# Kernel optimization log

Measured on AMD Instinct MI355X. Metric: run time of the kernel, lower is better.

## Reference

```python
import jax, jax.numpy as jnp
import numpy as np

N_MET, N_RXN, N_GENE = 2534, 4881, 6607
E, P, D = 262144, 131072, 256
LN_EPS = 1e-5


def _segment_mean(x, idx, n):
    s = jax.ops.segment_sum(x, idx, num_segments=n)
    c = jax.ops.segment_sum(jnp.ones((idx.shape[0],), x.dtype), idx, num_segments=n)
    return s / jnp.maximum(c, 1.0)[:, None]


def _hyperconv(x, eattr, node, edge, stoich, W, We, att, b):
    # PyG-style HypergraphConv with stoichiometry as incidence weight + attention.
    xp = x @ W                      # [N_MET, D]
    ep = eattr @ We                 # [N_RXN, D]
    xi = xp[node]                   # [E, D] gather
    ej = ep[edge]                   # [E, D] gather
    logits = jax.nn.leaky_relu(jnp.concatenate([xi, ej], axis=-1) @ att, 0.2)  # [E]
    m = jax.ops.segment_max(logits, edge, num_segments=N_RXN)
    ex = jnp.exp(logits - m[edge])
    ssum = jax.ops.segment_sum(ex, edge, num_segments=N_RXN)
    alpha = ex / (ssum[edge] + 1e-16)           # softmax per hyperedge
    w = stoich * alpha                           # [E]
    ones = jnp.ones_like(stoich)
    Bc = jax.ops.segment_sum(ones, edge, num_segments=N_RXN)   # nodes per edge
    me = jax.ops.segment_sum(w[:, None] * xi, edge, num_segments=N_RXN)
    me = me / jnp.maximum(Bc, 1.0)[:, None]      # node -> hyperedge
    Dc = jax.ops.segment_sum(ones, node, num_segments=N_MET)   # edges per node
    out = jax.ops.segment_sum(w[:, None] * me[edge], node, num_segments=N_MET)
    out = out / jnp.maximum(Dc, 1.0)[:, None]    # hyperedge -> node
    return out + b


def _layernorm(z, g, b):
    mu = jnp.mean(z, axis=-1, keepdims=True)
    var = jnp.mean(jnp.square(z - mu), axis=-1, keepdims=True)
    return (z - mu) / jnp.sqrt(var + LN_EPS) * g + b


def _renorm(emb):
    # nn.Embedding(max_norm=1.0): clamp row norms to <= 1
    n = jnp.linalg.norm(emb, axis=-1, keepdims=True)
    return emb * jnp.minimum(1.0, 1.0 / (n + 1e-12))


def setup_inputs() -> dict:
    key = jax.random.key(0)
    ks = jax.random.split(key, 16)
    s = 1.0 / np.sqrt(D)
    return {
        "he_node": jax.random.randint(ks[0], (E,), 0, N_MET),
        "he_edge": jax.random.randint(ks[1], (E,), 0, N_RXN),
        "stoich": jax.random.normal(ks[2], (E,), dtype=jnp.float32),
        "gene_x": jax.random.normal(ks[3], (N_GENE, D), dtype=jnp.float32),
        "rtg_rxn": jax.random.randint(ks[4], (P,), 0, N_RXN),
        "rtg_gene": jax.random.randint(ks[5], (P,), 0, N_GENE),
        "emb_table": jax.random.normal(ks[6], (N_MET, D), dtype=jnp.float32) * 0.02,
        "W0": jax.random.normal(ks[7], (D, D), dtype=jnp.float32) * s,
        "We0": jax.random.normal(ks[8], (D, D), dtype=jnp.float32) * s,
        "att0": jax.random.normal(ks[9], (2 * D,), dtype=jnp.float32) * s,
        "b0": jnp.zeros((D,), jnp.float32),
        "W1": jax.random.normal(ks[10], (D, D), dtype=jnp.float32) * s,
        "We1": jax.random.normal(ks[11], (D, D), dtype=jnp.float32) * s,
        "att1": jax.random.normal(ks[12], (2 * D,), dtype=jnp.float32) * s,
        "b1": jnp.zeros((D,), jnp.float32),
        "ln_g": jnp.ones((D,), jnp.float32),
        "ln_b": jnp.zeros((D,), jnp.float32),
    }


def reference(he_node, he_edge, stoich, gene_x, rtg_rxn, rtg_gene, emb_table,
              W0, We0, att0, b0, W1, We1, att1, b1, ln_g, ln_b):
    met = _renorm(emb_table)                                    # [N_MET, D]
    # gene -> reaction scatter-mean (flattened reaction_to_genes dict)
    rxn_emb = _segment_mean(gene_x[rtg_gene], rtg_rxn, N_RXN)   # [N_RXN, D]
    # layer 0 (no skip on first layer)
    cur = jnp.tanh(_hyperconv(met, rxn_emb, he_node, he_edge, stoich, W0, We0, att0, b0))
    # layer 1 with skip + layernorm
    nxt = jnp.tanh(_hyperconv(cur, rxn_emb, he_node, he_edge, stoich, W1, We1, att1, b1))
    cur = _layernorm(nxt + cur, ln_g, ln_b)
    # metabolite -> reaction scatter-mean over incidences
    rxn_final = _segment_mean(cur[he_node], he_edge, N_RXN)     # [N_RXN, D]
    # reaction -> gene scatter-mean
    gene_emb = _segment_mean(rxn_final[rtg_rxn], rtg_gene, N_GENE)  # [N_GENE, D]
    return gene_emb
```

## Files before the change

kernel.cpp:

```cpp
#include <hip/hip_runtime.h>
#include <math.h>

#define DD 256
static constexpr int N_MET  = 2534;
static constexpr int N_RXN  = 4881;
static constexpr int N_GENE = 6607;
static constexpr int NE     = 262144;
static constexpr int NP     = 131072;

static constexpr int NCHUNK = 256;
static constexpr int NCHG   = 128;
static constexpr int NBE    = 77;
static constexpr int NBN    = 80;
static constexpr int NBG    = 104;
static constexpr int CHS    = 80;
static constexpr int NCOL   = NBE + NBN + NBG;
static constexpr int GEMM_BLOCKS = (N_MET + 15) / 16;
static constexpr int KP2_GEMM0 = NBE + NBN + NBG;

__device__ __forceinline__ float waveSum(float v) {
  #pragma unroll
  for (int o = 32; o > 0; o >>= 1) v += __shfl_xor(v, o, 64);
  return v;
}
__device__ __forceinline__ float waveMax(float v) {
  #pragma unroll
  for (int o = 32; o > 0; o >>= 1) v = fmaxf(v, __shfl_xor(v, o, 64));
  return v;
}
__device__ __forceinline__ int   bcasti(int v, int l)   { return __builtin_amdgcn_readlane(v, l); }
__device__ __forceinline__ float bcastf(float v, int l) {
  return __int_as_float(__builtin_amdgcn_readlane(__float_as_int(v), l));
}

__global__ __launch_bounds__(1024) void KH_k(
    const int* __restrict__ he_node, const int* __restrict__ he_edge,
    const int* __restrict__ rtg_rxn, const int* __restrict__ rtg_gene,
    int* cntR,
    int* __restrict__ chE, int* __restrict__ chN, int* __restrict__ chG,
    const float* __restrict__ We0, const float* __restrict__ att0,
    const float* __restrict__ We1, const float* __restrict__ att1,
    float* __restrict__ ve0, float* __restrict__ ve1) {
  int blk = blockIdx.x, tid = threadIdx.x;
  if (blk < 32) {
    int wid = blk * 16 + (tid >> 6);
    int lane = tid & 63;
    const float* We = (wid < 256) ? We0 : We1;
    const float* at = (wid < 256) ? att0 : att1;
    int r = wid & 255;
    float4 a = ((const float4*)(We + (size_t)r * DD))[lane];
    float4 v = ((const float4*)(at + DD))[lane];
    float s = waveSum(a.x * v.x + a.y * v.y + a.z * v.z + a.w * v.w);
    if (lane == 0) ((wid < 256) ? ve0 : ve1)[r] = s;
    return;
  }
  int c = blk - 32;
  __shared__ int hE[NBE], hN[NBN], hG[NBG];
  if (tid < NBE) hE[tid] = 0;
  if (tid >= 128 && tid < 128 + NBN) hN[tid - 128] = 0;
  if (tid >= 256 && tid < 256 + NBG) hG[tid - 256] = 0;
  __syncthreads();
  int i = c * 1024 + tid;
  int n = he_node[i], e = he_edge[i];
  atomicAdd(&hE[e >> 6], 1); atomicAdd(&hN[n >> 5], 1);
  if (c < NCHG) {
    int r = rtg_rxn[i], g = rtg_gene[i];
    atomicAdd(&cntR[r], 1);
    atomicAdd(&hG[g >> 6], 1);
  }
  __syncthreads();
  if (tid < NBE) chE[c * CHS + tid] = hE[tid];
  if (tid >= 128 && tid < 128 + NBN) chN[c * CHS + (tid - 128)] = hN[tid - 128];
  if (c < NCHG && tid >= 256 && tid < 256 + NBG) chG[c * NBG + (tid - 256)] = hG[tid - 256];
}

__global__ __launch_bounds__(1024) void KScan_k(
    int* __restrict__ chE, int* __restrict__ chN, int* __restrict__ chG,
    int* __restrict__ totE, int* __restrict__ totN, int* __restrict__ totG,
    const float* __restrict__ gene_x,
    const float* __restrict__ ve0, const float* __restrict__ ve1,
    float* __restrict__ gdot0, float* __restrict__ gdot1) {
  int blk = blockIdx.x, tid = threadIdx.x;
  if (blk < 17) {
    int colw = blk * 16 + (tid >> 6);
    int lane = tid & 63;
// ... 52 lines not shown
}

__global__ __launch_bounds__(1024) void KP1_k(
    const int* __restrict__ he_node, const int* __restrict__ he_edge,
    const float* __restrict__ stoich,
    const int* __restrict__ chE, const int* __restrict__ chN,
    const int* __restrict__ chG,
    const int* __restrict__ totE, const int* __restrict__ totN,
    const int* __restrict__ totG,
    int2* __restrict__ scrE, int2* __restrict__ scrN, int* __restrict__ scrG,
    const int* __restrict__ rtg_rxn, const int* __restrict__ rtg_gene,
    const float* __restrict__ gdot0, const float* __restrict__ gdot1,
    float* __restrict__ seAcc0, float* __restrict__ seAcc1) {
  int c = blockIdx.x, tid = threadIdx.x;
  __shared__ int sc[128];
  __shared__ int cursE[NBE], cursN[NBN], cursG[NBG];
  int v;
  if (tid < 128) sc[tid] = (tid < NBE) ? totE[tid] : 0;
  if (tid < 128) v = sc[tid];
  __syncthreads();
  ldsScan128(sc, tid);
  if (tid < NBE) cursE[tid] = (sc[tid] - v) + chE[c * CHS + tid];
  __syncthreads();
  if (tid < 128) sc[tid] = (tid < NBN) ? totN[tid] : 0;
  if (tid < 128) v = sc[tid];
  __syncthreads();
  ldsScan128(sc, tid);
  if (tid < NBN) cursN[tid] = (sc[tid] - v) + chN[c * CHS + tid];
  __syncthreads();
  if (c < NCHG) {
    if (tid < 128) sc[tid] = (tid < NBG) ? totG[tid] : 0;
    if (tid < 128) v = sc[tid];
    __syncthreads();
    ldsScan128(sc, tid);
    if (tid < NBG) cursG[tid] = (sc[tid] - v) + chG[c * NBG + tid];
  }
  __syncthreads();
  int i = c * 1024 + tid;
  int n = he_node[i], e = he_edge[i];
  int st = __float_as_int(stoich[i]);
  int dE = atomicAdd(&cursE[e >> 6], 1);
  scrE[dE] = make_int2((e << 12) | n, st);
  int dN = atomicAdd(&cursN[n >> 5], 1);
  scrN[dN] = make_int2((n << 13) | e, st);
  if (c < NCHG) {
    int r = rtg_rxn[i], g = rtg_gene[i];
    int dG = atomicAdd(&cursG[g >> 6], 1);
    scrG[dG] = (g << 13) | r;
    atomicAdd(&seAcc0[r], gdot0[g]);
    atomicAdd(&seAcc1[r], gdot1[g]);
  }
}

template <bool RENORM>
__device__ __forceinline__ void gemm_body(const float* __restrict__ X,
                                          const float* __restrict__ W,
                                          const float* __restrict__ att,
                                          float* __restrict__ Y,
                                          float* __restrict__ sn, int M, int r0) {
  __shared__ float Xs[256][20];
  __shared__ float red[4][16];
  __shared__ float scl[16];
  int tid = threadIdx.x;
  int w = tid >> 6, lane = tid & 63;
  float xv[16];
  #pragma unroll
  for (int i = 0; i < 16; ++i) {
    int r = r0 + i;
    xv[i] = (r < M) ? X[(size_t)r * DD + tid] : 0.f;
  }
  if (RENORM) {
    #pragma unroll
    for (int i = 0; i < 16; ++i) {
      float v = waveSum(xv[i] * xv[i]);
      if (lane == 0) red[w][i] = v;
    }
    __syncthreads();
    if (tid < 16) {
      float t = red[0][tid] + red[1][tid] + red[2][tid] + red[3][tid];
      scl[tid] = fminf(1.f, 1.f / (sqrtf(t) + 1e-12f));
    }
    __syncthreads();
    #pragma unroll
    for (int i = 0; i < 16; ++i) xv[i] *= scl[i];
  }
  #pragma unroll
  for (int i = 0; i < 16; ++i) Xs[tid][i] = xv[i];
  __syncthreads();
  float acc[16];
  #pragma unroll
  for (int i = 0; i < 16; ++i) acc[i] = 0.f;
  const float* wp = W + tid;
  #pragma unroll 8
  for (int k = 0; k < 256; ++k) {
    float wv = wp[(size_t)k * DD];
    const float4* xr = reinterpret_cast<const float4*>(&Xs[k][0]);
    float4 a0 = xr[0], a1 = xr[1], a2 = xr[2], a3 = xr[3];
    acc[0]  += a0.x * wv; acc[1]  += a0.y * wv; acc[2]  += a0.z * wv; acc[3]  += a0.w * wv;
    acc[4]  += a1.x * wv; acc[5]  += a1.y * wv; acc[6]  += a1.z * wv; acc[7]  += a1.w * wv;
    acc[8]  += a2.x * wv; acc[9]  += a2.y * wv; acc[10] += a2.z * wv; acc[11] += a2.w * wv;
    acc[12] += a3.x * wv; acc[13] += a3.y * wv; acc[14] += a3.z * wv; acc[15] += a3.w * wv;
  }
  #pragma unroll
  for (int i = 0; i < 16; ++i) {
    int r = r0 + i;
    if (r < M) Y[(size_t)r * DD + tid] = acc[i];
  }
  float av = att[tid];
  __syncthreads();
  #pragma unroll
  for (int i = 0; i < 16; ++i) {
    float v = waveSum(acc[i] * av);
    if (lane == 0) red[w][i] = v;
  }
  __syncthreads();
  if (tid < 16) {
    int r = r0 + tid;
    if (r < M) sn[r] = red[0][tid] + red[1][tid] + red[2][tid] + red[3][tid];
  }
}

__device__ __forceinline__ int blockSumInt256(int v) {
  __shared__ int s4[4];
  #pragma unroll
  for (int o = 32; o > 0; o >>= 1) v += __shfl_xor(v, o, 64);
  if ((threadIdx.x & 63) == 0) s4[threadIdx.x >> 6] = v;
  __syncthreads();
  return s4[0] + s4[1] + s4[2] + s4[3];
}

__global__ __launch_bounds__(256) void KP2_k(
    const int* __restrict__ totE, const int* __restrict__ totN,
    const int* __restrict__ totG,
    const int2* __restrict__ scrE, const int2* __restrict__ scrN,
    const int* __restrict__ scrG,
    int* __restrict__ offsE, int* __restrict__ offsN, int* __restrict__ offsG,
    int2* __restrict__ payE, int2* __restrict__ payN, int* __restrict__ rxnG,
    const float* __restrict__ emb, const float* __restrict__ W0,
    const float* __restrict__ att0, float* __restrict__ xp, float* __restrict__ sn) {
  int blk = blockIdx.x, tid = threadIdx.x;
  if (blk >= KP2_GEMM0) {
    gemm_body<true>(emb, W0, att0, xp, sn, N_MET, (blk - KP2_GEMM0) * 16);
    return;
  }
  __shared__ int cnt[64];
  __shared__ int curs[64];
  int side, b, klo, kcnt, nk, btot;
  const int* tot;
  if (blk < NBE)            { side = 0; b = blk;             tot = totE; klo = 64 * b; nk = N_RXN;  kcnt = min(64, N_RXN  - klo); }
  else if (blk < NBE + NBN) { side = 1; b = blk - NBE;       tot = totN; klo = 32 * b; nk = N_MET;  kcnt = min(32, N_MET  - klo); }
  else                      { side = 2; b = blk - NBE - NBN; tot = totG; klo = 64 * b; nk = N_GENE; kcnt = min(64, N_GENE - klo); }
  btot = tot[b];
  int pv = (tid < b) ? tot[tid] : 0;
  int base = blockSumInt256(pv);
  if (tid < 64) cnt[tid] = 0;
  __syncthreads();
  int lo = base, hi = base + btot;
  for (int j = lo + tid; j < hi; j += 256) {
    int key;
    if (side == 0)      key = (scrE[j].x >> 12) - klo;
    else if (side == 1) key = (scrN[j].x >> 13) - klo;
    else                key = (scrG[j]   >> 13) - klo;
    atomicAdd(&cnt[key], 1);
  }
  __syncthreads();
  if (tid < 64) {
    int v = cnt[tid];
    int inc = v;
    #pragma unroll
    for (int o = 1; o < 64; o <<= 1) { int t = __shfl_up(inc, o, 64); if (tid >= o) inc += t; }
    int ex = inc - v;
    curs[tid] = base + ex;
    int* offs = (side == 0) ? offsE : (side == 1) ? offsN : offsG;
    if (tid < kcnt) offs[klo + tid] = base + ex;
    if (tid == 0 && klo + kcnt == nk) offs[nk] = base + btot;
  }
  __syncthreads();
  for (int j = lo + tid; j < hi; j += 256) {
    if (side == 0) {
      int2 r = scrE[j];
      int e = r.x >> 12, n = r.x & 4095;
      int slot = atomicAdd(&curs[e - klo], 1);
      payE[slot] = make_int2(n, r.y);
    } else if (side == 1) {
      int2 r = scrN[j];
      int n = r.x >> 13, e = r.x & 8191;
      int slot = atomicAdd(&curs[n - klo], 1);
      payN[slot] = make_int2(e, r.y);
    } else {
      int pw = scrG[j];
      int g = pw >> 13, rr = pw & 8191;
      int slot = atomicAdd(&curs[g - klo], 1);
      rxnG[slot] = rr;
    }
  }
}

__global__ __launch_bounds__(256) void gemm1_k(const float* __restrict__ X,
                                               const float* __restrict__ W,
                                               const float* __restrict__ att,
                                               float* __restrict__ Y,
                                               float* __restrict__ sn, int M) {
  gemm_body<false>(X, W, att, Y, sn, M, blockIdx.x * 16);
}

__device__ __forceinline__ void gatherAcc(float4& acc, const float4* __restrict__ src4,
                                          const int (&rv)[4], const float (&wv)[4],
                                          int nc, int lane) {
  #pragma unroll
  for (int c = 0; c < 4; ++c) {
    int lim = nc - c * 64; if (lim > 64) lim = 64;
    for (int t = 0; t < lim; t += 16) {
      float4 a[16]; float w[16];
      #pragma unroll
      for (int q = 0; q < 16; ++q) {
        int   n = bcasti(rv[c], t + q);
        w[q]    = bcastf(wv[c], t + q);
        a[q]    = src4[(size_t)n * 64 + lane];
      }
      #pragma unroll
      for (int q = 0; q < 16; ++q) {
        acc.x += w[q] * a[q].x; acc.y += w[q] * a[q].y;
        acc.z += w[q] * a[q].z; acc.w += w[q] * a[q].w;
      }
    }
  }
}

__device__ __forceinline__ void gatherAcc2(float2& acc, const float2* __restrict__ src2,
                                           const int (&rv)[4], const float (&wv)[4],
                                           int nc, int fbase) {
  #pragma unroll
  for (int c = 0; c < 4; ++c) {
    int lim = nc - c * 64; if (lim > 64) lim = 64;
    for (int t = 0; t < lim; t += 16) {
      float2 a[16]; float w[16];
      #pragma unroll
      for (int q = 0; q < 16; ++q) {
        int   n = bcasti(rv[c], t + q);
        w[q]    = bcastf(wv[c], t + q);
        a[q]    = src2[(size_t)n * 128 + fbase];
      }
      #pragma unroll
      for (int q = 0; q < 16; ++q) {
        acc.x += w[q] * a[q].x; acc.y += w[q] * a[q].y;
      }
    }
  }
}

template <int STRIDE>
__global__ __launch_bounds__(256) void seg_mean_k(const int* __restrict__ offs,
                                                  const int* __restrict__ pay,
                                                  const float* __restrict__ src,
                                                  float* __restrict__ dst, int nseg) {
  int wid = (blockIdx.x * 256 + threadIdx.x) >> 6;
  int lane = threadIdx.x & 63;
  if (wid >= nseg) return;
  int beg = offs[wid], end = offs[wid + 1];
  int cnt = end - beg;
  int nc = cnt < 256 ? cnt : 256;
  int rv[4]; float wv[4];
  #pragma unroll
  for (int c = 0; c < 4; ++c) {
    int j = c * 64 + lane;
    if (j < nc) { rv[c] = pay[(size_t)(beg + j) * STRIDE]; wv[c] = 1.f; }
    else        { rv[c] = 0;                               wv[c] = 0.f; }
  }
  float4 acc = make_float4(0.f, 0.f, 0.f, 0.f);
  gatherAcc(acc, (const float4*)src, rv, wv, nc, lane);
  for (int j = 256; j < cnt; ++j) {
    int n = pay[(size_t)(beg + j) * STRIDE];
    float4 a = ((const float4*)src)[(size_t)n * 64 + lane];
    acc.x += a.x; acc.y += a.y; acc.z += a.z; acc.w += a.w;
  }
  float inv = 1.f / (float)(cnt > 1 ? cnt : 1);
  float4 o; o.x = acc.x * inv; o.y = acc.y * inv; o.z = acc.z * inv; o.w = acc.w * inv;
  ((float4*)dst)[(size_t)wid * 64 + lane] = o;
}

__global__ __launch_bounds__(256) void me_k(const int* __restrict__ offs,
                                            const int2* __restrict__ payE,
                                            const float* __restrict__ sn,
                                            const float* __restrict__ seAcc,
                                            const int* __restrict__ cntR,
                                            const float* __restrict__ xp,
                                            float* __restrict__ me,
                                            float4* __restrict__ rstat) {
  int gw = (blockIdx.x * 256 + threadIdx.x) >> 6;
  int wid = gw >> 1, half = gw & 1;
  int lane = threadIdx.x & 63;
  if (wid >= N_RXN) return;
  int rc = cntR[wid];
  float ser = seAcc[wid] / (float)(rc > 1 ? rc : 1);

  int beg = offs[wid], end = offs[wid + 1];
  int cnt = end - beg;
  int nc = cnt < 256 ? cnt : 256;
  int nv[4]; float wv[4]; float stv[4];
  float lmax = -1e30f;
  #pragma unroll
  for (int c = 0; c < 4; ++c) {
    int j = c * 64 + lane;
    if (j < nc) {
      int2 p = payE[beg + j];
      float l = sn[p.x] + ser;
      l = (l >= 0.f) ? l : 0.2f * l;
      nv[c] = p.x; wv[c] = l; stv[c] = __int_as_float(p.y);
      lmax = fmaxf(lmax, l);
    } else { nv[c] = 0; wv[c] = -1e30f; stv[c] = 0.f; }
  }
  for (int j = 256 + lane; j < cnt; j += 64) {
    int2 p = payE[beg + j];
    float l = sn[p.x] + ser;
    l = (l >= 0.f) ? l : 0.2f * l;
    lmax = fmaxf(lmax, l);
  }
  float m = waveMax(lmax);
  float s = 0.f;
  #pragma unroll
  for (int c = 0; c < 4; ++c) {
    if (c * 64 + lane < nc) { float e = expf(wv[c] - m); wv[c] = e; s += e; }
    else wv[c] = 0.f;
  }
  for (int j = 256 + lane; j < cnt; j += 64) {
    int2 p = payE[beg + j];
    float l = sn[p.x] + ser;
    l = (l >= 0.f) ? l : 0.2f * l;
    s += expf(l - m);
  }
  s = waveSum(s);
  float invS = 1.f / (s + 1e-16f);
  #pragma unroll
  for (int c = 0; c < 4; ++c) {
    if (c * 64 + lane < nc) wv[c] = stv[c] * wv[c] * invS;
  }
  if (half == 0 && lane == 0) rstat[wid] = make_float4(ser, m, invS, 0.f);
  int fbase = half * 64 + lane;
  float2 acc = make_float2(0.f, 0.f);
  gatherAcc2(acc, (const float2*)xp, nv, wv, nc, fbase);
  for (int j = 256; j < cnt; ++j) {
    int2 p = payE[beg + j];
    float l = sn[p.x] + ser;
    l = (l >= 0.f) ? l : 0.2f * l;
    float w = __int_as_float(p.y) * expf(l - m) * invS;
    float2 a = ((const float2*)xp)[(size_t)p.x * 128 + fbase];
    acc.x += w * a.x; acc.y += w * a.y;
  }
  float invB = 1.f / (float)(cnt > 1 ? cnt : 1);
  float2 o; o.x = acc.x * invB; o.y = acc.y * invB;
  ((float2*)me)[(size_t)wid * 128 + fbase] = o;
}

template <bool LN>
__global__ __launch_bounds__(256) void out_k(const int* __restrict__ offs,
                                             const int2* __restrict__ payN,
                                             const float* __restrict__ sn,
                                             const float4* __restrict__ rstat,
                                             const float* __restrict__ me,
                                             const float* __restrict__ bias,
                                             const float* __restrict__ ln_g,
                                             const float* __restrict__ ln_b,
                                             float* __restrict__ cur) {
  int wid = (blockIdx.x * 256 + threadIdx.x) >> 6;
  int lane = threadIdx.x & 63;
  if (wid >= N_MET) return;
  int beg = offs[wid], end = offs[wid + 1];
  int cnt = end - beg;
  int nc = cnt < 256 ? cnt : 256;
  float sn_n = sn[wid];
  int rv[4]; float wv[4];
  #pragma unroll
  for (int c = 0; c < 4; ++c) {
    int j = c * 64 + lane;
    if (j < nc) {
      int2 p = payN[beg + j];
      float4 st = rstat[p.x];
      float l = sn_n + st.x;
      l = (l >= 0.f) ? l : 0.2f * l;
      rv[c] = p.x;
      wv[c] = __int_as_float(p.y) * expf(l - st.y) * st.z;
    } else { rv[c] = 0; wv[c] = 0.f; }
  }
  float4 acc = make_float4(0.f, 0.f, 0.f, 0.f);
  gatherAcc(acc, (const float4*)me, rv, wv, nc, lane);
  for (int j = 256; j < cnt; ++j) {
    int2 p = payN[beg + j];
    float4 st = rstat[p.x];
    float l = sn_n + st.x;
    l = (l >= 0.f) ? l : 0.2f * l;
    float w = __int_as_float(p.y) * expf(l - st.y) * st.z;
    float4 a = ((const float4*)me)[(size_t)p.x * 64 + lane];
    acc.x += w * a.x; acc.y += w * a.y; acc.z += w * a.z; acc.w += w * a.w;
  }
  float invD = 1.f / (float)(cnt > 1 ? cnt : 1);
  float4 b4 = ((const float4*)bias)[lane];
  float4 o;
  o.x = tanhf(acc.x * invD + b4.x);
  o.y = tanhf(acc.y * invD + b4.y);
  o.z = tanhf(acc.z * invD + b4.z);
  o.w = tanhf(acc.w * invD + b4.w);
  float4* cur4 = (float4*)cur;
  if (!LN) {
    cur4[(size_t)wid * 64 + lane] = o;
    return;
  }
  float4 p = cur4[(size_t)wid * 64 + lane];
  float4 z; z.x = o.x + p.x; z.y = o.y + p.y; z.z = o.z + p.z; z.w = o.w + p.w;
  float mu = waveSum(z.x + z.y + z.z + z.w) * (1.f / 256.f);
  float4 zc; zc.x = z.x - mu; zc.y = z.y - mu; zc.z = z.z - mu; zc.w = z.w - mu;
  float var = waveSum(zc.x * zc.x + zc.y * zc.y + zc.z * zc.z + zc.w * zc.w) * (1.f / 256.f);
  float rs = 1.f / sqrtf(var + 1e-5f);
  float4 g4 = ((const float4*)ln_g)[lane];
  float4 be4 = ((const float4*)ln_b)[lane];
  float4 r;
  r.x = zc.x * rs * g4.x + be4.x;
  r.y = zc.y * rs * g4.y + be4.y;
  r.z = zc.z * rs * g4.z + be4.z;
  r.w = zc.w * rs * g4.w + be4.w;
  cur4[(size_t)wid * 64 + lane] = r;
}

extern "C" void kernel_launch(void* const* d_in, const int* in_sizes, int n_in,
                              void* d_out, int out_size, void* d_ws, size_t ws_size,
                              hipStream_t stream) {
  const int*   he_node = (const int*)d_in[0];
  const int*   he_edge = (const int*)d_in[1];
  const float* stoich  = (const float*)d_in[2];
  const float* gene_x  = (const float*)d_in[3];
  const int*   rtg_rxn = (const int*)d_in[4];
  const int*   rtg_gene= (const int*)d_in[5];
  const float* emb     = (const float*)d_in[6];
  const float* W0      = (const float*)d_in[7];
  const float* We0     = (const float*)d_in[8];
  const float* att0    = (const float*)d_in[9];
  const float* b0      = (const float*)d_in[10];
  const float* W1      = (const float*)d_in[11];
  const float* We1     = (const float*)d_in[12];
  const float* att1    = (const float*)d_in[13];
  const float* b1      = (const float*)d_in[14];
  const float* ln_g    = (const float*)d_in[15];
  const float* ln_b    = (const float*)d_in[16];
  float* out = (float*)d_out;

  char* base = (char*)d_ws;
  size_t off = 0;
  auto carve = [&](size_t bytes) -> char* {
    char* p = base + off;
    off += (bytes + 255) & ~(size_t)255;
    return p;
  };
  float*  xp    = (float*)carve((size_t)N_MET * DD * 4);
  float*  me    = (float*)carve((size_t)N_RXN * DD * 4);
  float*  cur   = (float*)carve((size_t)N_MET * DD * 4);
  float*  rxnf  = (float*)carve((size_t)N_RXN * DD * 4);
  float*  sn    = (float*)carve((size_t)N_MET * 4);
  float*  ve0   = (float*)carve(DD * 4);
  float*  ve1   = (float*)carve(DD * 4);
  float*  gdot0 = (float*)carve((size_t)N_GENE * 4);
  float*  gdot1 = (float*)carve((size_t)N_GENE * 4);
  float4* rstat = (float4*)carve((size_t)N_RXN * 16);
  int ztot = 3 * N_RXN;
  int* zbase = (int*)carve((size_t)ztot * 4);
  int*   cntR   = zbase;
  float* seAcc0 = (float*)(cntR + N_RXN);
  float* seAcc1 = seAcc0 + N_RXN;
  int*  offsE = (int*)carve((N_RXN + 1) * 4);
  int2* payE  = (int2*)carve((size_t)NE * 8);
  int*  offsN = (int*)carve((N_MET + 1) * 4);
  int2* payN  = (int2*)carve((size_t)NE * 8);
  int*  offsG = (int*)carve((N_GENE + 1) * 4);
  int*  rxnG  = (int*)carve((size_t)NP * 4);
  int2* scrE  = (int2*)carve((size_t)NE * 8);
  int2* scrN  = (int2*)carve((size_t)NE * 8);
  int*  scrG  = (int*)carve((size_t)NP * 4);
  int*  chE   = (int*)carve((size_t)NCHUNK * CHS * 4);
  int*  chN   = (int*)carve((size_t)NCHUNK * CHS * 4);
  int*  chG   = (int*)carve((size_t)NCHG * NBG * 4);
  int*  totE  = (int*)carve(128 * 4);
  int*  totN  = (int*)carve(128 * 4);
  int*  totG  = (int*)carve(128 * 4);

  hipMemsetAsync(zbase, 0, (size_t)ztot * 4, stream);

  KH_k<<<32 + NCHUNK, 1024, 0, stream>>>(
      he_node, he_edge, rtg_rxn, rtg_gene, cntR,
      chE, chN, chG, We0, att0, We1, att1, ve0, ve1);

  int gdot_blocks = (N_GENE + 15) / 16;
  KScan_k<<<17 + gdot_blocks, 1024, 0, stream>>>(
      chE, chN, chG, totE, totN, totG, gene_x, ve0, ve1, gdot0, gdot1);

  KP1_k<<<NCHUNK, 1024, 0, stream>>>(
      he_node, he_edge, stoich, chE, chN, chG, totE, totN, totG,
      scrE, scrN, scrG, rtg_rxn, rtg_gene, gdot0, gdot1, seAcc0, seAcc1);

  KP2_k<<<KP2_GEMM0 + GEMM_BLOCKS, 256, 0, stream>>>(
      totE, totN, totG, scrE, scrN, scrG,
      offsE, offsN, offsG, payE, payN, rxnG,
      emb, W0, att0, xp, sn);

  me_k<<<(2 * N_RXN + 3) / 4, 256, 0, stream>>>(offsE, payE, sn, seAcc0, cntR,
                                                xp, me, rstat);
  out_k<false><<<(N_MET + 3) / 4, 256, 0, stream>>>(offsN, payN, sn, rstat, me, b0,
                                                    nullptr, nullptr, cur);

  gemm1_k<<<GEMM_BLOCKS, 256, 0, stream>>>(cur, W1, att1, xp, sn, N_MET);
  me_k<<<(2 * N_RXN + 3) / 4, 256, 0, stream>>>(offsE, payE, sn, seAcc1, cntR,
                                                xp, me, rstat);
  out_k<true><<<(N_MET + 3) / 4, 256, 0, stream>>>(offsN, payN, sn, rstat, me, b1,
                                                   ln_g, ln_b, cur);

  seg_mean_k<2><<<(N_RXN + 3) / 4, 256, 0, stream>>>(offsE, (const int*)payE, cur, rxnf, N_RXN);
  seg_mean_k<1><<<(N_GENE + 3) / 4, 256, 0, stream>>>(offsG, rxnG, rxnf, out, N_GENE);
}
```

Baseline: 221.8 us.

## Assign one block per segment and split incidences across four waves

```diff
diff --git a/kernel.cpp b/kernel.cpp
--- a/kernel.cpp
+++ b/kernel.cpp
@@ -31,6 +31,22 @@
 __device__ __forceinline__ int   bcasti(int v, int l)   { return __builtin_amdgcn_readlane(v, l); }
 __device__ __forceinline__ float bcastf(float v, int l) {
   return __int_as_float(__builtin_amdgcn_readlane(__float_as_int(v), l));
+}
+__device__ __forceinline__ float blockMax4(float v, float* red, int w, int lane) {
+  v = waveMax(v);
+  if (lane == 0) red[w] = v;
+  __syncthreads();
+  float r = fmaxf(fmaxf(red[0], red[1]), fmaxf(red[2], red[3]));
+  __syncthreads();
+  return r;
+}
+__device__ __forceinline__ float blockSum4(float v, float* red, int w, int lane) {
+  v = waveSum(v);
+  if (lane == 0) red[w] = v;
+  __syncthreads();
+  float r = red[0] + red[1] + red[2] + red[3];
+  __syncthreads();
+  return r;
 }
 
 __global__ __launch_bounds__(1024) void KH_k(
@@ -341,12 +357,12 @@
   gemm_body<false>(X, W, att, Y, sn, M, blockIdx.x * 16);
 }
 
-__device__ __forceinline__ void gatherAcc(float4& acc, const float4* __restrict__ src4,
-                                          const int (&rv)[4], const float (&wv)[4],
-                                          int nc, int lane) {
+__device__ __forceinline__ void gatherWave(float4& acc, const float4* __restrict__ src4,
+                                           const int (&rv)[4], const float (&wv)[4],
+                                           int jn, int lane) {
   #pragma unroll
   for (int c = 0; c < 4; ++c) {
-    int lim = nc - c * 64; if (lim > 64) lim = 64;
+    int lim = jn - c * 64; if (lim > 64) lim = 64;
     for (int t = 0; t < lim; t += 16) {
       float4 a[16]; float w[16];
       #pragma unroll
@@ -364,154 +380,124 @@
   }
 }
 
-__device__ __forceinline__ void gatherAcc2(float2& acc, const float2* __restrict__ src2,
-                                           const int (&rv)[4], const float (&wv)[4],
-                                           int nc, int fbase) {
-  #pragma unroll
-  for (int c = 0; c < 4; ++c) {
-    int lim = nc - c * 64; if (lim > 64) lim = 64;
-    for (int t = 0; t < lim; t += 16) {
-      float2 a[16]; float w[16];
-      #pragma unroll
-      for (int q = 0; q < 16; ++q) {
-        int   n = bcasti(rv[c], t + q);
-        w[q]    = bcastf(wv[c], t + q);
-        a[q]    = src2[(size_t)n * 128 + fbase];
-      }
-      #pragma unroll
-      for (int q = 0; q < 16; ++q) {
-        acc.x += w[q] * a[q].x; acc.y += w[q] * a[q].y;
-      }
-    }
-  }
-}
-
-template <int STRIDE>
-__global__ __launch_bounds__(256) void seg_mean_k(const int* __restrict__ offs,
-                                                  const int* __restrict__ pay,
-                                                  const float* __restrict__ src,
-                                                  float* __restrict__ dst, int nseg) {
-  int wid = (blockIdx.x * 256 + threadIdx.x) >> 6;
-  int lane = threadIdx.x & 63;
-  if (wid >= nseg) return;
-  int beg = offs[wid], end = offs[wid + 1];
+__device__ __forceinline__ bool combine4(float4& acc, float4 (*lacc)[64], int w, int lane) {
+  if (w > 0) lacc[w - 1][lane] = acc;
+  __syncthreads();
+  if (w == 0) {
+    float4 a1 = lacc[0][lane], a2 = lacc[1][lane], a3 = lacc[2][lane];
+    acc.x += a1.x + a2.x + a3.x;
+    acc.y += a1.y + a2.y + a3.y;
+    acc.z += a1.z + a2.z + a3.z;
+    acc.w += a1.w + a2.w + a3.w;
+    return true;
+  }
+  return false;
+}
+
+__global__ __launch_bounds__(256) void me_blk_k(const int* __restrict__ offs,
+                                                const int2* __restrict__ payE,
+                                                const float* __restrict__ sn,
+                                                const float* __restrict__ seAcc,
+                                                const int* __restrict__ cntR,
+                                                const float* __restrict__ xp,
+                                                float* __restrict__ me,
+                                                float4* __restrict__ rstat) {
+  __shared__ float red[4];
+  __shared__ float4 lacc[3][64];
+  int r = blockIdx.x;
+  int tid = threadIdx.x, w = tid >> 6, lane = tid & 63;
+  int beg = offs[r], end = offs[r + 1];
   int cnt = end - beg;
-  int nc = cnt < 256 ? cnt : 256;
-  int rv[4]; float wv[4];
+  int rc = cntR[r];
+  float ser = seAcc[r] / (float)(rc > 1 ? rc : 1);
+  int cap = cnt < 1024 ? cnt : 1024;
+  int q = (cap + 3) >> 2;
+  int jb = w * q;
+  int jn = cap - jb; if (jn < 0) jn = 0; if (jn > q) jn = q;
+  int nv[4]; float wv[4], stv[4];
+  float lmax = -1e30f;
   #pragma unroll
   for (int c = 0; c < 4; ++c) {
     int j = c * 64 + lane;
-    if (j < nc) { rv[c] = pay[(size_t)(beg + j) * STRIDE]; wv[c] = 1.f; }
-    else        { rv[c] = 0;                               wv[c] = 0.f; }
-  }
-  float4 acc = make_float4(0.f, 0.f, 0.f, 0.f);
-  gatherAcc(acc, (const float4*)src, rv, wv, nc, lane);
-  for (int j = 256; j < cnt; ++j) {
-    int n = pay[(size_t)(beg + j) * STRIDE];
-    float4 a = ((const float4*)src)[(size_t)n * 64 + lane];
-    acc.x += a.x; acc.y += a.y; acc.z += a.z; acc.w += a.w;
-  }
-  float inv = 1.f / (float)(cnt > 1 ? cnt : 1);
-  float4 o; o.x = acc.x * inv; o.y = acc.y * inv; o.z = acc.z * inv; o.w = acc.w * inv;
-  ((float4*)dst)[(size_t)wid * 64 + lane] = o;
-}
-
-__global__ __launch_bounds__(256) void me_k(const int* __restrict__ offs,
-                                            const int2* __restrict__ payE,
-                                            const float* __restrict__ sn,
-                                            const float* __restrict__ seAcc,
-                                            const int* __restrict__ cntR,
-                                            const float* __restrict__ xp,
-                                            float* __restrict__ me,
-                                            float4* __restrict__ rstat) {
-  int gw = (blockIdx.x * 256 + threadIdx.x) >> 6;
-  int wid = gw >> 1, half = gw & 1;
-  int lane = threadIdx.x & 63;
-  if (wid >= N_RXN) return;
-  int rc = cntR[wid];
-  float ser = seAcc[wid] / (float)(rc > 1 ? rc : 1);
-
-  int beg = offs[wid], end = offs[wid + 1];
-  int cnt = end - beg;
-  int nc = cnt < 256 ? cnt : 256;
-  int nv[4]; float wv[4]; float stv[4];
-  float lmax = -1e30f;
-  #pragma unroll
-  for (int c = 0; c < 4; ++c) {
-    int j = c * 64 + lane;
-    if (j < nc) {
-      int2 p = payE[beg + j];
+    if (j < jn) {
+      int2 p = payE[beg + jb + j];
       float l = sn[p.x] + ser;
       l = (l >= 0.f) ? l : 0.2f * l;
       nv[c] = p.x; wv[c] = l; stv[c] = __int_as_float(p.y);
       lmax = fmaxf(lmax, l);
     } else { nv[c] = 0; wv[c] = -1e30f; stv[c] = 0.f; }
   }
-  for (int j = 256 + lane; j < cnt; j += 64) {
+  for (int j = 1024 + tid; j < cnt; j += 256) {
     int2 p = payE[beg + j];
     float l = sn[p.x] + ser;
     l = (l >= 0.f) ? l : 0.2f * l;
     lmax = fmaxf(lmax, l);
   }
-  float m = waveMax(lmax);
+  float m = blockMax4(lmax, red, w, lane);
   float s = 0.f;
   #pragma unroll
   for (int c = 0; c < 4; ++c) {
-    if (c * 64 + lane < nc) { float e = expf(wv[c] - m); wv[c] = e; s += e; }
+    if (c * 64 + lane < jn) { float e = expf(wv[c] - m); wv[c] = e; s += e; }
     else wv[c] = 0.f;
   }
-  for (int j = 256 + lane; j < cnt; j += 64) {
+  for (int j = 1024 + tid; j < cnt; j += 256) {
     int2 p = payE[beg + j];
     float l = sn[p.x] + ser;
     l = (l >= 0.f) ? l : 0.2f * l;
     s += expf(l - m);
   }
-  s = waveSum(s);
-  float invS = 1.f / (s + 1e-16f);
+  float S = blockSum4(s, red, w, lane);
+  float invS = 1.f / (S + 1e-16f);
   #pragma unroll
   for (int c = 0; c < 4; ++c) {
-    if (c * 64 + lane < nc) wv[c] = stv[c] * wv[c] * invS;
-  }
-  if (half == 0 && lane == 0) rstat[wid] = make_float4(ser, m, invS, 0.f);
-  int fbase = half * 64 + lane;
-  float2 acc = make_float2(0.f, 0.f);
-  gatherAcc2(acc, (const float2*)xp, nv, wv, nc, fbase);
-  for (int j = 256; j < cnt; ++j) {
-    int2 p = payE[beg + j];
-    float l = sn[p.x] + ser;
-    l = (l >= 0.f) ? l : 0.2f * l;
-    float w = __int_as_float(p.y) * expf(l - m) * invS;
-    float2 a = ((const float2*)xp)[(size_t)p.x * 128 + fbase];
-    acc.x += w * a.x; acc.y += w * a.y;
-  }
-  float invB = 1.f / (float)(cnt > 1 ? cnt : 1);
-  float2 o; o.x = acc.x * invB; o.y = acc.y * invB;
-  ((float2*)me)[(size_t)wid * 128 + fbase] = o;
+    if (c * 64 + lane < jn) wv[c] = stv[c] * wv[c] * invS;
+  }
+  if (tid == 0) rstat[r] = make_float4(ser, m, invS, 0.f);
+  float4 acc = make_float4(0.f, 0.f, 0.f, 0.f);
+  gatherWave(acc, (const float4*)xp, nv, wv, jn, lane);
+  if (w == 0) {
+    for (int j = 1024; j < cnt; ++j) {
+      int2 p = payE[beg + j];
+      float l = sn[p.x] + ser;
+      l = (l >= 0.f) ? l : 0.2f * l;
+      float ww = __int_as_float(p.y) * expf(l - m) * invS;
+      float4 a = ((const float4*)xp)[(size_t)p.x * 64 + lane];
+      acc.x += ww * a.x; acc.y += ww * a.y; acc.z += ww * a.z; acc.w += ww * a.w;
+    }
+  }
+  if (combine4(acc, lacc, w, lane)) {
+    float invB = 1.f / (float)(cnt > 1 ? cnt : 1);
+    float4 o; o.x = acc.x * invB; o.y = acc.y * invB; o.z = acc.z * invB; o.w = acc.w * invB;
+    ((float4*)me)[(size_t)r * 64 + lane] = o;
+  }
 }
 
 template <bool LN>
-__global__ __launch_bounds__(256) void out_k(const int* __restrict__ offs,
-                                             const int2* __restrict__ payN,
-                                             const float* __restrict__ sn,
-                                             const float4* __restrict__ rstat,
-                                             const float* __restrict__ me,
-                                             const float* __restrict__ bias,
-                                             const float* __restrict__ ln_g,
-                                             const float* __restrict__ ln_b,
-                                             float* __restrict__ cur) {
-  int wid = (blockIdx.x * 256 + threadIdx.x) >> 6;
-  int lane = threadIdx.x & 63;
-  if (wid >= N_MET) return;
-  int beg = offs[wid], end = offs[wid + 1];
+__global__ __launch_bounds__(256) void out_blk_k(const int* __restrict__ offs,
+                                                 const int2* __restrict__ payN,
+                                                 const float* __restrict__ sn,
+                                                 const float4* __restrict__ rstat,
+                                                 const float* __restrict__ me,
+                                                 const float* __restrict__ bias,
+                                                 const float* __restrict__ ln_g,
+                                                 const float* __restrict__ ln_b,
+                                                 float* __restrict__ cur) {
+  __shared__ float4 lacc[3][64];
+  int n = blockIdx.x;
+  int tid = threadIdx.x, w = tid >> 6, lane = tid & 63;
+  int beg = offs[n], end = offs[n + 1];
   int cnt = end - beg;
-  int nc = cnt < 256 ? cnt : 256;
-  float sn_n = sn[wid];
+  float sn_n = sn[n];
+  int cap = cnt < 1024 ? cnt : 1024;
+  int q = (cap + 3) >> 2;
+  int jb = w * q;
+  int jn = cap - jb; if (jn < 0) jn = 0; if (jn > q) jn = q;
   int rv[4]; float wv[4];
   #pragma unroll
   for (int c = 0; c < 4; ++c) {
     int j = c * 64 + lane;
-    if (j < nc) {
-      int2 p = payN[beg + j];
+    if (j < jn) {
+      int2 p = payN[beg + jb + j];
       float4 st = rstat[p.x];
       float l = sn_n + st.x;
       l = (l >= 0.f) ? l : 0.2f * l;
@@ -520,16 +506,19 @@
     } else { rv[c] = 0; wv[c] = 0.f; }
   }
   float4 acc = make_float4(0.f, 0.f, 0.f, 0.f);
-  gatherAcc(acc, (const float4*)me, rv, wv, nc, lane);
-  for (int j = 256; j < cnt; ++j) {
-    int2 p = payN[beg + j];
-    float4 st = rstat[p.x];
-    float l = sn_n + st.x;
-    l = (l >= 0.f) ? l : 0.2f * l;
-    float w = __int_as_float(p.y) * expf(l - st.y) * st.z;
-    float4 a = ((const float4*)me)[(size_t)p.x * 64 + lane];
-    acc.x += w * a.x; acc.y += w * a.y; acc.z += w * a.z; acc.w += w * a.w;
-  }
+  gatherWave(acc, (const float4*)me, rv, wv, jn, lane);
+  if (w == 0) {
+    for (int j = 1024; j < cnt; ++j) {
+      int2 p = payN[beg + j];
+      float4 st = rstat[p.x];
+      float l = sn_n + st.x;
+      l = (l >= 0.f) ? l : 0.2f * l;
+      float ww = __int_as_float(p.y) * expf(l - st.y) * st.z;
+      float4 a = ((const float4*)me)[(size_t)p.x * 64 + lane];
+      acc.x += ww * a.x; acc.y += ww * a.y; acc.z += ww * a.z; acc.w += ww * a.w;
+    }
+  }
+  if (!combine4(acc, lacc, w, lane)) return;
   float invD = 1.f / (float)(cnt > 1 ? cnt : 1);
   float4 b4 = ((const float4*)bias)[lane];
   float4 o;
@@ -539,10 +528,10 @@
   o.w = tanhf(acc.w * invD + b4.w);
   float4* cur4 = (float4*)cur;
   if (!LN) {
-    cur4[(size_t)wid * 64 + lane] = o;
+    cur4[(size_t)n * 64 + lane] = o;
     return;
   }
-  float4 p = cur4[(size_t)wid * 64 + lane];
+  float4 p = cur4[(size_t)n * 64 + lane];
   float4 z; z.x = o.x + p.x; z.y = o.y + p.y; z.z = o.z + p.z; z.w = o.w + p.w;
   float mu = waveSum(z.x + z.y + z.z + z.w) * (1.f / 256.f);
   float4 zc; zc.x = z.x - mu; zc.y = z.y - mu; zc.z = z.z - mu; zc.w = z.w - mu;
@@ -550,12 +539,49 @@
   float rs = 1.f / sqrtf(var + 1e-5f);
   float4 g4 = ((const float4*)ln_g)[lane];
   float4 be4 = ((const float4*)ln_b)[lane];
-  float4 r;
-  r.x = zc.x * rs * g4.x + be4.x;
-  r.y = zc.y * rs * g4.y + be4.y;
-  r.z = zc.z * rs * g4.z + be4.z;
-  r.w = zc.w * rs * g4.w + be4.w;
-  cur4[(size_t)wid * 64 + lane] = r;
+  float4 rr;
+  rr.x = zc.x * rs * g4.x + be4.x;
+  rr.y = zc.y * rs * g4.y + be4.y;
+  rr.z = zc.z * rs * g4.z + be4.z;
+  rr.w = zc.w * rs * g4.w + be4.w;
+  cur4[(size_t)n * 64 + lane] = rr;
+}
+
+template <int STRIDE>
+__global__ __launch_bounds__(256) void segmean_blk_k(const int* __restrict__ offs,
+                                                     const int* __restrict__ pay,
+                                                     const float* __restrict__ src,
+                                                     float* __restrict__ dst) {
+  __shared__ float4 lacc[3][64];
+  int sgm = blockIdx.x;
+  int tid = threadIdx.x, w = tid >> 6, lane = tid & 63;
+  int beg = offs[sgm], end = offs[sgm + 1];
+  int cnt = end - beg;
+  int cap = cnt < 1024 ? cnt : 1024;
+  int q = (cap + 3) >> 2;
+  int jb = w * q;
+  int jn = cap - jb; if (jn < 0) jn = 0; if (jn > q) jn = q;
+  int rv[4]; float wv[4];
+  #pragma unroll
+  for (int c = 0; c < 4; ++c) {
+    int j = c * 64 + lane;
+    if (j < jn) { rv[c] = pay[(size_t)(beg + jb + j) * STRIDE]; wv[c] = 1.f; }
+    else        { rv[c] = 0;                                    wv[c] = 0.f; }
+  }
+  float4 acc = make_float4(0.f, 0.f, 0.f, 0.f);
+  gatherWave(acc, (const float4*)src, rv, wv, jn, lane);
+  if (w == 0) {
+    for (int j = 1024; j < cnt; ++j) {
+      int g = pay[(size_t)(beg + j) * STRIDE];
+      float4 a = ((const float4*)src)[(size_t)g * 64 + lane];
+      acc.x += a.x; acc.y += a.y; acc.z += a.z; acc.w += a.w;
+    }
+  }
+  if (combine4(acc, lacc, w, lane)) {
+    float inv = 1.f / (float)(cnt > 1 ? cnt : 1);
+    float4 o; o.x = acc.x * inv; o.y = acc.y * inv; o.z = acc.z * inv; o.w = acc.w * inv;
+    ((float4*)dst)[(size_t)sgm * 64 + lane] = o;
+  }
 }
 
 extern "C" void kernel_launch(void* const* d_in, const int* in_sizes, int n_in,
@@ -637,17 +663,15 @@
       offsE, offsN, offsG, payE, payN, rxnG,
       emb, W0, att0, xp, sn);
 
-  me_k<<<(2 * N_RXN + 3) / 4, 256, 0, stream>>>(offsE, payE, sn, seAcc0, cntR,
-                                                xp, me, rstat);
-  out_k<false><<<(N_MET + 3) / 4, 256, 0, stream>>>(offsN, payN, sn, rstat, me, b0,
-                                                    nullptr, nullptr, cur);
+  me_blk_k<<<N_RXN, 256, 0, stream>>>(offsE, payE, sn, seAcc0, cntR, xp, me, rstat);
+  out_blk_k<false><<<N_MET, 256, 0, stream>>>(offsN, payN, sn, rstat, me, b0,
+                                              nullptr, nullptr, cur);
 
   gemm1_k<<<GEMM_BLOCKS, 256, 0, stream>>>(cur, W1, att1, xp, sn, N_MET);
-  me_k<<<(2 * N_RXN + 3) / 4, 256, 0, stream>>>(offsE, payE, sn, seAcc1, cntR,
-                                                xp, me, rstat);
-  out_k<true><<<(N_MET + 3) / 4, 256, 0, stream>>>(offsN, payN, sn, rstat, me, b1,
-                                                   ln_g, ln_b, cur);
-
-  seg_mean_k<2><<<(N_RXN + 3) / 4, 256, 0, stream>>>(offsE, (const int*)payE, cur, rxnf, N_RXN);
-  seg_mean_k<1><<<(N_GENE + 3) / 4, 256, 0, stream>>>(offsG, rxnG, rxnf, out, N_GENE);
-}
+  me_blk_k<<<N_RXN, 256, 0, stream>>>(offsE, payE, sn, seAcc1, cntR, xp, me, rstat);
+  out_blk_k<true><<<N_MET, 256, 0, stream>>>(offsN, payN, sn, rstat, me, b1,
+                                             ln_g, ln_b, cur);
+
+  segmean_blk_k<2><<<N_RXN, 256, 0, stream>>>(offsE, (const int*)payE, cur, rxnf);
+  segmean_blk_k<1><<<N_GENE, 256, 0, stream>>>(offsG, rxnG, rxnf, out);
+}
```

Result: slower. 228.5 us (+3.0%).

## Store intermediate feature matrices in fp16 with scaling for gather kernels

Applied to the files above, without the earlier changes.

```diff
diff --git a/kernel.cpp b/kernel.cpp
--- a/kernel.cpp
+++ b/kernel.cpp
@@ -1,4 +1,5 @@
 #include <hip/hip_runtime.h>
+#include <hip/hip_fp16.h>
 #include <math.h>
 
 #define DD 256
@@ -18,6 +19,9 @@
 static constexpr int GEMM_BLOCKS = (N_MET + 15) / 16;
 static constexpr int KP2_GEMM0 = NBE + NBN + NBG;
 
+static constexpr float SCL  = 2048.f;
+static constexpr float SCLI = 1.f / 2048.f;
+
 __device__ __forceinline__ float waveSum(float v) {
   #pragma unroll
   for (int o = 32; o > 0; o >>= 1) v += __shfl_xor(v, o, 64);
@@ -31,6 +35,21 @@
 __device__ __forceinline__ int   bcasti(int v, int l)   { return __builtin_amdgcn_readlane(v, l); }
 __device__ __forceinline__ float bcastf(float v, int l) {
   return __int_as_float(__builtin_amdgcn_readlane(__float_as_int(v), l));
+}
+
+__device__ __forceinline__ float4 h4f(uint2 u) {
+  __half2 a = *reinterpret_cast<__half2*>(&u.x);
+  __half2 b = *reinterpret_cast<__half2*>(&u.y);
+  float2 fa = __half22float2(a), fb = __half22float2(b);
+  return make_float4(fa.x, fa.y, fb.x, fb.y);
+}
+__device__ __forceinline__ uint2 f4h(float4 v) {
+  __half2 a = __floats2half2_rn(v.x, v.y);
+  __half2 b = __floats2half2_rn(v.z, v.w);
+  uint2 u;
+  u.x = *reinterpret_cast<unsigned*>(&a);
+  u.y = *reinterpret_cast<unsigned*>(&b);
+  return u;
 }
 
 __global__ __launch_bounds__(1024) void KH_k(
@@ -189,11 +208,11 @@
   }
 }
 
-template <bool RENORM>
-__device__ __forceinline__ void gemm_body(const float* __restrict__ X,
+template <bool RENORM, bool XH>
+__device__ __forceinline__ void gemm_body(const void* __restrict__ Xv,
                                           const float* __restrict__ W,
                                           const float* __restrict__ att,
-                                          float* __restrict__ Y,
+                                          __half* __restrict__ Y,
                                           float* __restrict__ sn, int M, int r0) {
   __shared__ float Xs[256][20];
   __shared__ float red[4][16];
@@ -204,7 +223,10 @@
   #pragma unroll
   for (int i = 0; i < 16; ++i) {
     int r = r0 + i;
-    xv[i] = (r < M) ? X[(size_t)r * DD + tid] : 0.f;
+    if (r < M) {
+      if (XH) xv[i] = __half2float(((const __half*)Xv)[(size_t)r * DD + tid]);
+      else    xv[i] = ((const float*)Xv)[(size_t)r * DD + tid];
+    } else xv[i] = 0.f;
   }
   if (RENORM) {
     #pragma unroll
@@ -238,10 +260,11 @@
     acc[8]  += a2.x * wv; acc[9]  += a2.y * wv; acc[10] += a2.z * wv; acc[11] += a2.w * wv;
     acc[12] += a3.x * wv; acc[13] += a3.y * wv; acc[14] += a3.z * wv; acc[15] += a3.w * wv;
   }
+  const float ysc = XH ? 1.f : SCL;
   #pragma unroll
   for (int i = 0; i < 16; ++i) {
     int r = r0 + i;
-    if (r < M) Y[(size_t)r * DD + tid] = acc[i];
+    if (r < M) Y[(size_t)r * DD + tid] = __float2half_rn(acc[i] * ysc);
   }
   float av = att[tid];
   __syncthreads();
@@ -253,7 +276,8 @@
   __syncthreads();
   if (tid < 16) {
     int r = r0 + tid;
-    if (r < M) sn[r] = red[0][tid] + red[1][tid] + red[2][tid] + red[3][tid];
+    if (r < M) sn[r] = (red[0][tid] + red[1][tid] + red[2][tid] + red[3][tid])
+                       * (XH ? SCLI : 1.f);
   }
 }
 
@@ -274,10 +298,11 @@
     int* __restrict__ offsE, int* __restrict__ offsN, int* __restrict__ offsG,
     int2* __restrict__ payE, int2* __restrict__ payN, int* __restrict__ rxnG,
     const float* __restrict__ emb, const float* __restrict__ W0,
-    const float* __restrict__ att0, float* __restrict__ xp, float* __restrict__ sn) {
+    const float* __restrict__ att0, __half* __restrict__ xp,
+    float* __restrict__ sn) {
   int blk = blockIdx.x, tid = threadIdx.x;
   if (blk >= KP2_GEMM0) {
-    gemm_body<true>(emb, W0, att0, xp, sn, N_MET, (blk - KP2_GEMM0) * 16);
+    gemm_body<true, false>(emb, W0, att0, xp, sn, N_MET, (blk - KP2_GEMM0) * 16);
     return;
   }
   __shared__ int cnt[64];
@@ -333,64 +358,43 @@
   }
 }
 
-__global__ __launch_bounds__(256) void gemm1_k(const float* __restrict__ X,
+__global__ __launch_bounds__(256) void gemm1_k(const __half* __restrict__ X,
                                                const float* __restrict__ W,
                                                const float* __restrict__ att,
-                                               float* __restrict__ Y,
+                                               __half* __restrict__ Y,
                                                float* __restrict__ sn, int M) {
-  gemm_body<false>(X, W, att, Y, sn, M, blockIdx.x * 16);
-}
-
-__device__ __forceinline__ void gatherAcc(float4& acc, const float4* __restrict__ src4,
-                                          const int (&rv)[4], const float (&wv)[4],
-                                          int nc, int lane) {
+  gemm_body<false, true>(X, W, att, Y, sn, M, blockIdx.x * 16);
+}
+
+__device__ __forceinline__ void gatherAccH(float4& acc, const uint2* __restrict__ src,
+                                           const int (&rv)[4], const float (&wv)[4],
+                                           int nc, int lane) {
   #pragma unroll
   for (int c = 0; c < 4; ++c) {
     int lim = nc - c * 64; if (lim > 64) lim = 64;
     for (int t = 0; t < lim; t += 16) {
-      float4 a[16]; float w[16];
+      uint2 a[16]; float w[16];
       #pragma unroll
       for (int q = 0; q < 16; ++q) {
         int   n = bcasti(rv[c], t + q);
         w[q]    = bcastf(wv[c], t + q);
-        a[q]    = src4[(size_t)n * 64 + lane];
+        a[q]    = src[(size_t)n * 64 + lane];
       }
       #pragma unroll
       for (int q = 0; q < 16; ++q) {
-        acc.x += w[q] * a[q].x; acc.y += w[q] * a[q].y;
-        acc.z += w[q] * a[q].z; acc.w += w[q] * a[q].w;
+        float4 f = h4f(a[q]);
+        acc.x += w[q] * f.x; acc.y += w[q] * f.y;
+        acc.z += w[q] * f.z; acc.w += w[q] * f.w;
       }
     }
   }
 }
 
-__device__ __forceinline__ void gatherAcc2(float2& acc, const float2* __restrict__ src2,
-                                           const int (&rv)[4], const float (&wv)[4],
-                                           int nc, int fbase) {
-  #pragma unroll
-  for (int c = 0; c < 4; ++c) {
-    int lim = nc - c * 64; if (lim > 64) lim = 64;
-    for (int t = 0; t < lim; t += 16) {
-      float2 a[16]; float w[16];
-      #pragma unroll
-      for (int q = 0; q < 16; ++q) {
-        int   n = bcasti(rv[c], t + q);
-        w[q]    = bcastf(wv[c], t + q);
-        a[q]    = src2[(size_t)n * 128 + fbase];
-      }
-      #pragma unroll
-      for (int q = 0; q < 16; ++q) {
-        acc.x += w[q] * a[q].x; acc.y += w[q] * a[q].y;
-      }
-    }
-  }
-}
-
-template <int STRIDE>
+template <int STRIDE, bool F32OUT>
 __global__ __launch_bounds__(256) void seg_mean_k(const int* __restrict__ offs,
                                                   const int* __restrict__ pay,
-                                                  const float* __restrict__ src,
-                                                  float* __restrict__ dst, int nseg) {
+                                                  const uint2* __restrict__ src,
+                                                  void* __restrict__ dst, int nseg) {
   int wid = (blockIdx.x * 256 + threadIdx.x) >> 6;
   int lane = threadIdx.x & 63;
   if (wid >= nseg) return;
@@ -405,15 +409,20 @@
     else        { rv[c] = 0;                               wv[c] = 0.f; }
   }
   float4 acc = make_float4(0.f, 0.f, 0.f, 0.f);
-  gatherAcc(acc, (const float4*)src, rv, wv, nc, lane);
+  gatherAccH(acc, src, rv, wv, nc, lane);
   for (int j = 256; j < cnt; ++j) {
     int n = pay[(size_t)(beg + j) * STRIDE];
-    float4 a = ((const float4*)src)[(size_t)n * 64 + lane];
+    float4 a = h4f(src[(size_t)n * 64 + lane]);
     acc.x += a.x; acc.y += a.y; acc.z += a.z; acc.w += a.w;
   }
   float inv = 1.f / (float)(cnt > 1 ? cnt : 1);
   float4 o; o.x = acc.x * inv; o.y = acc.y * inv; o.z = acc.z * inv; o.w = acc.w * inv;
-  ((float4*)dst)[(size_t)wid * 64 + lane] = o;
+  if (F32OUT) {
+    o.x *= SCLI; o.y *= SCLI; o.z *= SCLI; o.w *= SCLI;
+    ((float4*)dst)[(size_t)wid * 64 + lane] = o;
+  } else {
+    ((uint2*)dst)[(size_t)wid * 64 + lane] = f4h(o);
+  }
 }
 
 __global__ __launch_bounds__(256) void me_k(const int* __restrict__ offs,
@@ -421,11 +430,10 @@
                                             const float* __restrict__ sn,
                                             const float* __restrict__ seAcc,
                                             const int* __restrict__ cntR,
-                                            const float* __restrict__ xp,
-                                            float* __restrict__ me,
+                                            const uint2* __restrict__ xp,
+                                            uint2* __restrict__ me,
                                             float4* __restrict__ rstat) {
-  int gw = (blockIdx.x * 256 + threadIdx.x) >> 6;
-  int wid = gw >> 1, half = gw & 1;
+  int wid = (blockIdx.x * 256 + threadIdx.x) >> 6;
   int lane = threadIdx.x & 63;
   if (wid >= N_RXN) return;
   int rc = cntR[wid];
@@ -472,21 +480,20 @@
   for (int c = 0; c < 4; ++c) {
     if (c * 64 + lane < nc) wv[c] = stv[c] * wv[c] * invS;
   }
-  if (half == 0 && lane == 0) rstat[wid] = make_float4(ser, m, invS, 0.f);
-  int fbase = half * 64 + lane;
-  float2 acc = make_float2(0.f, 0.f);
-  gatherAcc2(acc, (const float2*)xp, nv, wv, nc, fbase);
+  if (lane == 0) rstat[wid] = make_float4(ser, m, invS, 0.f);
+  float4 acc = make_float4(0.f, 0.f, 0.f, 0.f);
+  gatherAccH(acc, xp, nv, wv, nc, lane);
   for (int j = 256; j < cnt; ++j) {
     int2 p = payE[beg + j];
     float l = sn[p.x] + ser;
     l = (l >= 0.f) ? l : 0.2f * l;
     float w = __int_as_float(p.y) * expf(l - m) * invS;
-    float2 a = ((const float2*)xp)[(size_t)p.x * 128 + fbase];
-    acc.x += w * a.x; acc.y += w * a.y;
+    float4 a = h4f(xp[(size_t)p.x * 64 + lane]);
+    acc.x += w * a.x; acc.y += w * a.y; acc.z += w * a.z; acc.w += w * a.w;
   }
   float invB = 1.f / (float)(cnt > 1 ? cnt : 1);
-  float2 o; o.x = acc.x * invB; o.y = acc.y * invB;
-  ((float2*)me)[(size_t)wid * 128 + fbase] = o;
+  float4 o; o.x = acc.x * invB; o.y = acc.y * invB; o.z = acc.z * invB; o.w = acc.w * invB;
+  me[(size_t)wid * 64 + lane] = f4h(o);
 }
 
 template <bool LN>
@@ -494,11 +501,11 @@
                                              const int2* __restrict__ payN,
                                              const float* __restrict__ sn,
                                              const float4* __restrict__ rstat,
-                                             const float* __restrict__ me,
+                                             const uint2* __restrict__ me,
                                              const float* __restrict__ bias,
                                              const float* __restrict__ ln_g,
                                              const float* __restrict__ ln_b,
-                                             float* __restrict__ cur) {
+                                             uint2* __restrict__ cur) {
   int wid = (blockIdx.x * 256 + threadIdx.x) >> 6;
   int lane = threadIdx.x & 63;
   if (wid >= N_MET) return;
@@ -520,29 +527,30 @@
     } else { rv[c] = 0; wv[c] = 0.f; }
   }
   float4 acc = make_float4(0.f, 0.f, 0.f, 0.f);
-  gatherAcc(acc, (const float4*)me, rv, wv, nc, lane);
+  gatherAccH(acc, me, rv, wv, nc, lane);
   for (int j = 256; j < cnt; ++j) {
     int2 p = payN[beg + j];
     float4 st = rstat[p.x];
     float l = sn_n + st.x;
     l = (l >= 0.f) ? l : 0.2f * l;
     float w = __int_as_float(p.y) * expf(l - st.y) * st.z;
-    float4 a = ((const float4*)me)[(size_t)p.x * 64 + lane];
+    float4 a = h4f(me[(size_t)p.x * 64 + lane]);
     acc.x += w * a.x; acc.y += w * a.y; acc.z += w * a.z; acc.w += w * a.w;
   }
-  float invD = 1.f / (float)(cnt > 1 ? cnt : 1);
+  float invD = SCLI / (float)(cnt > 1 ? cnt : 1);
   float4 b4 = ((const float4*)bias)[lane];
   float4 o;
   o.x = tanhf(acc.x * invD + b4.x);
   o.y = tanhf(acc.y * invD + b4.y);
   o.z = tanhf(acc.z * invD + b4.z);
   o.w = tanhf(acc.w * invD + b4.w);
-  float4* cur4 = (float4*)cur;
   if (!LN) {
-    cur4[(size_t)wid * 64 + lane] = o;
+    float4 so; so.x = o.x * SCL; so.y = o.y * SCL; so.z = o.z * SCL; so.w = o.w * SCL;
+    cur[(size_t)wid * 64 + lane] = f4h(so);
     return;
   }
-  float4 p = cur4[(size_t)wid * 64 + lane];
+  float4 p = h4f(cur[(size_t)wid * 64 + lane]);
+  p.x *= SCLI; p.y *= SCLI; p.z *= SCLI; p.w *= SCLI;
   float4 z; z.x = o.x + p.x; z.y = o.y + p.y; z.z = o.z + p.z; z.w = o.w + p.w;
   float mu = waveSum(z.x + z.y + z.z + z.w) * (1.f / 256.f);
   float4 zc; zc.x = z.x - mu; zc.y = z.y - mu; zc.z = z.z - mu; zc.w = z.w - mu;
@@ -551,11 +559,11 @@
   float4 g4 = ((const float4*)ln_g)[lane];
   float4 be4 = ((const float4*)ln_b)[lane];
   float4 r;
-  r.x = zc.x * rs * g4.x + be4.x;
-  r.y = zc.y * rs * g4.y + be4.y;
-  r.z = zc.z * rs * g4.z + be4.z;
-  r.w = zc.w * rs * g4.w + be4.w;
-  cur4[(size_t)wid * 64 + lane] = r;
+  r.x = (zc.x * rs * g4.x + be4.x) * SCL;
+  r.y = (zc.y * rs * g4.y + be4.y) * SCL;
+  r.z = (zc.z * rs * g4.z + be4.z) * SCL;
+  r.w = (zc.w * rs * g4.w + be4.w) * SCL;
+  cur[(size_t)wid * 64 + lane] = f4h(r);
 }
 
 extern "C" void kernel_launch(void* const* d_in, const int* in_sizes, int n_in,
@@ -587,10 +595,10 @@
     off += (bytes + 255) & ~(size_t)255;
     return p;
   };
-  float*  xp    = (float*)carve((size_t)N_MET * DD * 4);
-  float*  me    = (float*)carve((size_t)N_RXN * DD * 4);
-  float*  cur   = (float*)carve((size_t)N_MET * DD * 4);
-  float*  rxnf  = (float*)carve((size_t)N_RXN * DD * 4);
+  __half* xp_h   = (__half*)carve((size_t)N_MET * DD * 2);
+  __half* me_h   = (__half*)carve((size_t)N_RXN * DD * 2);
+  __half* cur_h  = (__half*)carve((size_t)N_MET * DD * 2);
+  __half* rxnf_h = (__half*)carve((size_t)N_RXN * DD * 2);
   float*  sn    = (float*)carve((size_t)N_MET * 4);
   float*  ve0   = (float*)carve(DD * 4);
   float*  ve1   = (float*)carve(DD * 4);
@@ -635,19 +643,23 @@
   KP2_k<<<KP2_GEMM0 + GEMM_BLOCKS, 256, 0, stream>>>(
       totE, totN, totG, scrE, scrN, scrG,
       offsE, offsN, offsG, payE, payN, rxnG,
-      emb, W0, att0, xp, sn);
-
-  me_k<<<(2 * N_RXN + 3) / 4, 256, 0, stream>>>(offsE, payE, sn, seAcc0, cntR,
-                                                xp, me, rstat);
-  out_k<false><<<(N_MET + 3) / 4, 256, 0, stream>>>(offsN, payN, sn, rstat, me, b0,
-                                                    nullptr, nullptr, cur);
-
-  gemm1_k<<<GEMM_BLOCKS, 256, 0, stream>>>(cur, W1, att1, xp, sn, N_MET);
-  me_k<<<(2 * N_RXN + 3) / 4, 256, 0, stream>>>(offsE, payE, sn, seAcc1, cntR,
-                                                xp, me, rstat);
-  out_k<true><<<(N_MET + 3) / 4, 256, 0, stream>>>(offsN, payN, sn, rstat, me, b1,
-                                                   ln_g, ln_b, cur);
-
-  seg_mean_k<2><<<(N_RXN + 3) / 4, 256, 0, stream>>>(offsE, (const int*)payE, cur, rxnf, N_RXN);
-  seg_mean_k<1><<<(N_GENE + 3) / 4, 256, 0, stream>>>(offsG, rxnG, rxnf, out, N_GENE);
-}
+      emb, W0, att0, xp_h, sn);
+
+  me_k<<<(N_RXN + 3) / 4, 256, 0, stream>>>(offsE, payE, sn, seAcc0, cntR,
+                                            (const uint2*)xp_h, (uint2*)me_h, rstat);
+  out_k<false><<<(N_MET + 3) / 4, 256, 0, stream>>>(offsN, payN, sn, rstat,
+                                                    (const uint2*)me_h, b0,
+                                                    nullptr, nullptr, (uint2*)cur_h);
+
+  gemm1_k<<<GEMM_BLOCKS, 256, 0, stream>>>(cur_h, W1, att1, xp_h, sn, N_MET);
+  me_k<<<(N_RXN + 3) / 4, 256, 0, stream>>>(offsE, payE, sn, seAcc1, cntR,
+                                            (const uint2*)xp_h, (uint2*)me_h, rstat);
+  out_k<true><<<(N_MET + 3) / 4, 256, 0, stream>>>(offsN, payN, sn, rstat,
+                                                   (const uint2*)me_h, b1,
+                                                   ln_g, ln_b, (uint2*)cur_h);
+
+  seg_mean_k<2, false><<<(N_RXN + 3) / 4, 256, 0, stream>>>(
+      offsE, (const int*)payE, (const uint2*)cur_h, rxnf_h, N_RXN);
+  seg_mean_k<1, true><<<(N_GENE + 3) / 4, 256, 0, stream>>>(
+      offsG, rxnG, (const uint2*)rxnf_h, out, N_GENE);
+}
```

New measurement: 198.0 us (median of 2 runs). 1.12x faster.
